# Kernel tuning notes

Hardware: AMD Instinct MI355X
Metric: run time of the kernel (lower is better)

## Reference

```python
import jax, jax.numpy as jnp
import numpy as np

EPS = 1e-9

def dice(x, alpha):
    # Dice: batch-norm over dim 0 (unbiased var, ddof=1), then gated blend.
    mu = jnp.mean(x, axis=0)
    var = jnp.var(x, axis=0, ddof=1)
    p = jax.nn.sigmoid((x - mu) / jnp.sqrt(var + EPS))
    return alpha * x * (1.0 - p) + x * p


def setup_inputs() -> dict:
    key = jax.random.key(0)
    ks = jax.random.split(key, 8)
    bs, seq, dim = 2048, 200, 64
    d_in = dim * 4
    return {
        "query": jax.random.normal(ks[0], (bs, dim), jnp.float32),
        "user_behavior": jax.random.normal(ks[1], (bs, seq, dim), jnp.float32),
        "mask": jax.random.uniform(ks[2], (bs, seq, 1), jnp.float32),
        "W1": jax.random.normal(ks[3], (d_in, 32), jnp.float32) / np.sqrt(d_in),
        "b1": jnp.zeros((32,), jnp.float32),
        "alpha1": jnp.zeros((1,), jnp.float32),
        "W2": jax.random.normal(ks[4], (32, 16), jnp.float32) / np.sqrt(32.0),
        "b2": jnp.zeros((16,), jnp.float32),
        "alpha2": jnp.zeros((1,), jnp.float32),
        "W3": jax.random.normal(ks[5], (16, 1), jnp.float32) / np.sqrt(16.0),
        "b3": jnp.zeros((1,), jnp.float32),
    }


def reference(query, user_behavior, mask, W1, b1, alpha1, W2, b2, alpha2, W3, b3):
    # query: (bs, dim) -> broadcast to (bs, seq, dim)
    q = jnp.broadcast_to(query[:, None, :], user_behavior.shape)
    attn_input = jnp.concatenate(
        [q, user_behavior, q - user_behavior, q * user_behavior], axis=-1
    )  # (bs, seq, 4*dim)
    h = dice(attn_input @ W1 + b1, alpha1)
    h = dice(h @ W2 + b2, alpha2)
    attns = h @ W3 + b3  # (bs, seq, 1)
    attns = attns * mask
    output = jnp.sum(user_behavior * attns, axis=1)  # (bs, dim)
    return output, attns
```

## Files before the change

kernel.cpp:

```cpp
#include <hip/hip_runtime.h>
#include <math.h>

#define BS  2048
#define SEQ 200
#define DIM 64
#define C1  32
#define C2  16

typedef __attribute__((ext_vector_type(8))) short bf16x8_t;
typedef __attribute__((ext_vector_type(4))) float f32x4_t;
typedef __attribute__((ext_vector_type(4))) short short4_t;

__device__ __forceinline__ float dice1(float x, float m, float r, float al) {
    float t = (x - m) * r;
    float p = 1.f / (1.f + __expf(-t));
    return x * (al + p * (1.f - al));
}

__device__ __forceinline__ unsigned short f2bf(float f) {
    union { float f; unsigned u; } a;
    a.f = f;
    unsigned r = a.u + 0x7fff + ((a.u >> 16) & 1);
    return (unsigned short)(r >> 16);
}

__global__ __launch_bounds__(256) void k_gemm1(const float* __restrict__ q,
                                               const float* __restrict__ ub,
                                               const float* __restrict__ W1,
                                               const float* __restrict__ b1,
                                               float* __restrict__ z1) {
    const int bs = blockIdx.x;
    const int tid = threadIdx.x;
    __shared__ __align__(16) short s_A[208 * 64];
    __shared__ __align__(16) short s_B[2 * 2 * 64 * 8];
    __shared__ __align__(16) float s_qw[C1];

    char* sAc = (char*)s_A;
    const float* qrow = q + bs * DIM;
    const float4* src4 = (const float4*)(ub + (size_t)bs * SEQ * DIM);

    float4 st[13];
    #pragma unroll
    for (int it = 0; it < 13; ++it) {
        int i = tid + it * 256;
        if (it < 12 || i < SEQ * 16) st[it] = src4[i];
        else { st[it].x = 0.f; st[it].y = 0.f; st[it].z = 0.f; st[it].w = 0.f; }
    }

    {
        const int kt = tid >> 7;
        const int nt = (tid >> 6) & 1;
        const int l  = tid & 63;
        const int c  = nt * 16 + (l & 15);
        bf16x8_t bfr;
        #pragma unroll
        for (int j = 0; j < 8; ++j) {
            int k = kt * 32 + ((l >> 4) << 3) + j;
            float wb = W1[(64 + k) * C1 + c] - W1[(128 + k) * C1 + c]
                     + qrow[k] * W1[(192 + k) * C1 + c];
            bfr[j] = (short)f2bf(wb);
        }
        *(bf16x8_t*)((char*)s_B + (((kt * 2 + nt) * 64) + l) * 16) = bfr;
    }
    if (tid < C1) {
        float a = b1[tid];
        #pragma unroll 8
        for (int d = 0; d < DIM; ++d)
            a = fmaf(qrow[d], W1[d * C1 + tid] + W1[(128 + d) * C1 + tid], a);
        s_qw[tid] = a;
    }

    #pragma unroll
    for (int it = 0; it < 13; ++it) {
        int i = tid + it * 256;
        int row = i >> 4, f4 = i & 15;
        int off = row * 128 + ((f4 * 8) ^ ((row & 7) << 4));
        short4_t u;
        u.x = (short)f2bf(st[it].x);
        u.y = (short)f2bf(st[it].y);
        u.z = (short)f2bf(st[it].z);
        u.w = (short)f2bf(st[it].w);
        *(short4_t*)(sAc + off) = u;
    }
    __syncthreads();

    const int wave = tid >> 6;
    const int l = tid & 63;
    const int g = l >> 4;
    const bf16x8_t b00 = *(const bf16x8_t*)((char*)s_B + (0 * 64 + l) * 16);
    const bf16x8_t b01 = *(const bf16x8_t*)((char*)s_B + (1 * 64 + l) * 16);
    const bf16x8_t b10 = *(const bf16x8_t*)((char*)s_B + (2 * 64 + l) * 16);
    const bf16x8_t b11 = *(const bf16x8_t*)((char*)s_B + (3 * 64 + l) * 16);
    const float qw0 = s_qw[l & 15];
    const float qw1 = s_qw[16 + (l & 15)];
    float* z1_b = z1 + (size_t)bs * SEQ * C1;

    for (int mt = wave; mt < 13; mt += 4) {
        const int row = mt * 16 + (l & 15);
        const int sw = (row & 7) << 4;
        bf16x8_t a0 = *(const bf16x8_t*)(sAc + row * 128 + ((g * 16) ^ sw));
        bf16x8_t a1 = *(const bf16x8_t*)(sAc + row * 128 + (((64 + g * 16)) ^ sw));
        f32x4_t acc0 = {0.f, 0.f, 0.f, 0.f};
        f32x4_t acc1 = {0.f, 0.f, 0.f, 0.f};
        acc0 = __builtin_amdgcn_mfma_f32_16x16x32_bf16(a0, b00, acc0, 0, 0, 0);
        acc0 = __builtin_amdgcn_mfma_f32_16x16x32_bf16(a1, b10, acc0, 0, 0, 0);
        acc1 = __builtin_amdgcn_mfma_f32_16x16x32_bf16(a0, b01, acc1, 0, 0, 0);
        acc1 = __builtin_amdgcn_mfma_f32_16x16x32_bf16(a1, b11, acc1, 0, 0, 0);
        const int orow = mt * 16 + g * 4;
        #pragma unroll
        for (int r = 0; r < 4; ++r) {
            int rr = orow + r;
            if (rr < SEQ) {
                z1_b[rr * C1 + (l & 15)]      = acc0[r] + qw0;
                z1_b[rr * C1 + 16 + (l & 15)] = acc1[r] + qw1;
            }
        }
    }
}

template <int C>
__global__ __launch_bounds__(256) void k_redA(const float* __restrict__ z,
                                              float* __restrict__ pS,
                                              float* __restrict__ pQ) {
    constexpr int Q = C / 4;
    constexpr int NG = 256 / Q;
    const int seq = blockIdx.x;
    const int part = blockIdx.y;
    const int cq = threadIdx.x % Q;
    const int g = threadIdx.x / Q;
    float4 s = {0.f, 0.f, 0.f, 0.f}, ss = {0.f, 0.f, 0.f, 0.f};
    const int b0 = part * 256;
    for (int b = b0 + g; b < b0 + 256; b += NG) {
        float4 v = *(const float4*)(z + ((size_t)b * SEQ + seq) * C + cq * 4);
        s.x += v.x; s.y += v.y; s.z += v.z; s.w += v.w;
        ss.x = fmaf(v.x, v.x, ss.x);
        ss.y = fmaf(v.y, v.y, ss.y);
        ss.z = fmaf(v.z, v.z, ss.z);
        ss.w = fmaf(v.w, v.w, ss.w);
    }
    __shared__ __align__(16) float4 sh_s[256];
    __shared__ __align__(16) float4 sh_q[256];
    sh_s[threadIdx.x] = s;
    sh_q[threadIdx.x] = ss;
    for (int h = NG / 2; h > 0; h >>= 1) {
        __syncthreads();
        if (g < h) {
            int o = threadIdx.x + h * Q;
            float4 s2 = sh_s[o], q2 = sh_q[o];
            s.x += s2.x; s.y += s2.y; s.z += s2.z; s.w += s2.w;
            ss.x += q2.x; ss.y += q2.y; ss.z += q2.z; ss.w += q2.w;
            sh_s[threadIdx.x] = s;
            sh_q[threadIdx.x] = ss;
        }
    }
    if (g == 0) {
        *(float4*)(pS + ((size_t)part * SEQ + seq) * C + cq * 4) = s;
        *(float4*)(pQ + ((size_t)part * SEQ + seq) * C + cq * 4) = ss;
    }
}

template <int C>
__global__ __launch_bounds__(64) void k_redB(const float* __restrict__ pS,
                                             const float* __restrict__ pQ,
                                             float* __restrict__ mu,
                                             float* __restrict__ rstd) {
    const int seq = blockIdx.x;
    const int c = threadIdx.x;
    if (c >= C) return;
    float s = 0.f, ss = 0.f;
    #pragma unroll
    for (int p = 0; p < 8; ++p) {
        s += pS[((size_t)p * SEQ + seq) * C + c];
        ss += pQ[((size_t)p * SEQ + seq) * C + c];
    }
    float m = s / (float)BS;
    float var = (ss - s * m) / (float)(BS - 1);
    mu[seq * C + c] = m;
    rstd[seq * C + c] = rsqrtf(var + 1e-9f);
}

__global__ __launch_bounds__(256) void k_gemm2(const float* __restrict__ z1,
                                               const float* __restrict__ mu1,
                                               const float* __restrict__ rstd1,
                                               const float* __restrict__ alpha1,
                                               const float* __restrict__ W2,
                                               const float* __restrict__ b2,
                                               float* __restrict__ z2) {
    const int tid = threadIdx.x;
    __shared__ __align__(16) float s_w2[C1 * C2];
    __shared__ float s_b2[C2];
    for (int i = tid; i < C1 * C2; i += 256) s_w2[i] = W2[i];
    if (tid < C2) s_b2[tid] = b2[tid];
    __syncthreads();
    const int gidx = blockIdx.x * 256 + tid;
    const int bsb = gidx / SEQ;
    const int seq = gidx - bsb * SEQ;
    const float al = alpha1[0];
    const float4* z4 = (const float4*)(z1 + (size_t)gidx * C1);
    const float4* m4 = (const float4*)(mu1 + seq * C1);
    const float4* r4 = (const float4*)(rstd1 + seq * C1);
    float h[C1];
    #pragma unroll
    for (int k = 0; k < C1 / 4; ++k) {
        float4 x = z4[k], m = m4[k], r = r4[k];
        h[k * 4 + 0] = dice1(x.x, m.x, r.x, al);
        h[k * 4 + 1] = dice1(x.y, m.y, r.y, al);
        h[k * 4 + 2] = dice1(x.z, m.z, r.z, al);
        h[k * 4 + 3] = dice1(x.w, m.w, r.w, al);
    }
    const float4* w4 = (const float4*)s_w2;
    float4 o[4];
    #pragma unroll
    for (int qd = 0; qd < 4; ++qd) {
        o[qd].x = s_b2[qd * 4 + 0];
        o[qd].y = s_b2[qd * 4 + 1];
        o[qd].z = s_b2[qd * 4 + 2];
        o[qd].w = s_b2[qd * 4 + 3];
    }
    #pragma unroll
    for (int c = 0; c < C1; ++c) {
        float hc = h[c];
        #pragma unroll
        for (int qd = 0; qd < 4; ++qd) {
            float4 w = w4[c * 4 + qd];
            o[qd].x = fmaf(hc, w.x, o[qd].x);
            o[qd].y = fmaf(hc, w.y, o[qd].y);
            o[qd].z = fmaf(hc, w.z, o[qd].z);
            o[qd].w = fmaf(hc, w.w, o[qd].w);
        }
    }
    float4* outp = (float4*)(z2 + (size_t)gidx * C2);
    #pragma unroll
    for (int qd = 0; qd < 4; ++qd) outp[qd] = o[qd];
}

__global__ __launch_bounds__(256) void k_final(const float* __restrict__ z2,
                                               const float* __restrict__ mu2,
                                               const float* __restrict__ rstd2,
                                               const float* __restrict__ alpha2,
                                               const float* __restrict__ W3,
                                               const float* __restrict__ b3,
                                               const float* __restrict__ mask,
                                               const float* __restrict__ ub,
                                               float* __restrict__ out,
                                               float* __restrict__ attns) {
    const int bs = blockIdx.x;
    const int tid = threadIdx.x;
    __shared__ float s_attn[SEQ];
    __shared__ float s_w3[C2];
    __shared__ __align__(16) float4 s_pool[256];
    if (tid < C2) s_w3[tid] = W3[tid];
    __syncthreads();
    if (tid < SEQ) {
        const float al = alpha2[0];
        const float bb3 = b3[0];
        const float4* z4 = (const float4*)(z2 + ((size_t)bs * SEQ + tid) * C2);
        const float4* m4 = (const float4*)(mu2 + tid * C2);
        const float4* r4 = (const float4*)(rstd2 + tid * C2);
        float a = bb3;
        #pragma unroll
        for (int k = 0; k < C2 / 4; ++k) {
            float4 x = z4[k], m = m4[k], r = r4[k];
            a = fmaf(dice1(x.x, m.x, r.x, al), s_w3[k * 4 + 0], a);
            a = fmaf(dice1(x.y, m.y, r.y, al), s_w3[k * 4 + 1], a);
            a = fmaf(dice1(x.z, m.z, r.z, al), s_w3[k * 4 + 2], a);
            a = fmaf(dice1(x.w, m.w, r.w, al), s_w3[k * 4 + 3], a);
        }
        a *= mask[bs * SEQ + tid];
        s_attn[tid] = a;
        attns[(size_t)bs * SEQ + tid] = a;
    }
    __syncthreads();
    const int dq = tid & 15;
    const int sg = tid >> 4;
    float4 acc = {0.f, 0.f, 0.f, 0.f};
    const float4* ub4 = (const float4*)(ub + (size_t)bs * SEQ * DIM);
    for (int s = sg; s < SEQ; s += 16) {
        float a = s_attn[s];
        float4 v = ub4[s * 16 + dq];
        acc.x = fmaf(v.x, a, acc.x);
        acc.y = fmaf(v.y, a, acc.y);
        acc.z = fmaf(v.z, a, acc.z);
        acc.w = fmaf(v.w, a, acc.w);
    }
    s_pool[tid] = acc;
    for (int h = 8; h > 0; h >>= 1) {
        __syncthreads();
        if (sg < h) {
            float4 o = s_pool[tid + h * 16];
            acc.x += o.x; acc.y += o.y; acc.z += o.z; acc.w += o.w;
            s_pool[tid] = acc;
        }
    }
    if (sg == 0)
        *(float4*)(out + (size_t)bs * DIM + dq * 4) = acc;
}

extern "C" void kernel_launch(void* const* d_in, const int* in_sizes, int n_in,
                              void* d_out, int out_size, void* d_ws, size_t ws_size,
                              hipStream_t stream) {
    const float* q    = (const float*)d_in[0];
    const float* ub   = (const float*)d_in[1];
    const float* mask = (const float*)d_in[2];
    const float* W1   = (const float*)d_in[3];
    const float* b1   = (const float*)d_in[4];
    const float* a1   = (const float*)d_in[5];
    const float* W2   = (const float*)d_in[6];
    const float* b2   = (const float*)d_in[7];
    const float* a2   = (const float*)d_in[8];
    const float* W3   = (const float*)d_in[9];
    const float* b3   = (const float*)d_in[10];

    float* out   = (float*)d_out;
    float* attns = out + (size_t)BS * DIM;

    float* ws = (float*)d_ws;
    float* z1 = ws;
    float* z2 = z1 + (size_t)BS * SEQ * C1;
    float* mu1   = z2 + (size_t)BS * SEQ * C2;
    float* rstd1 = mu1 + SEQ * C1;
    float* mu2   = rstd1 + SEQ * C1;
    float* rstd2 = mu2 + SEQ * C2;
    float* pS    = attns;
    float* pQ    = pS + 8 * SEQ * C1;

    hipLaunchKernelGGL(k_gemm1, dim3(BS), dim3(256), 0, stream, q, ub, W1, b1, z1);
    hipLaunchKernelGGL((k_redA<C1>), dim3(SEQ, 8), dim3(256), 0, stream, z1, pS, pQ);
    hipLaunchKernelGGL((k_redB<C1>), dim3(SEQ), dim3(64), 0, stream, pS, pQ, mu1, rstd1);
    hipLaunchKernelGGL(k_gemm2, dim3(BS * SEQ / 256), dim3(256), 0, stream, z1, mu1, rstd1, a1, W2, b2, z2);
    hipLaunchKernelGGL((k_redA<C2>), dim3(SEQ, 8), dim3(256), 0, stream, z2, pS, pQ);
    hipLaunchKernelGGL((k_redB<C2>), dim3(SEQ), dim3(64), 0, stream, pS, pQ, mu2, rstd2);
    hipLaunchKernelGGL(k_final, dim3(BS), dim3(256), 0, stream, z2, mu2, rstd2, a2, W3, b3, mask, ub, out, attns);
}
```

Baseline: 272.7 us.

## Store intermediates in bf16, fuse layer-2 GEMM with stat reductions, drop LDS staging

Intermediates z1 and z2 are now stored as bf16 instead of fp32, halving the traffic of the reduction and GEMM passes that re-read them. k_gemm1 reads user_behavior straight from global memory into MFMA fragments and writes its output tile through LDS with coalesced stores. The second GEMM moves to MFMA and is fused with the finalize step for layer-1 statistics and the partial sums for layer-2 statistics, which removes two kernel launches and one full pass over z2. In exchange, rounding to bf16 before the batch-norm statistics adds precision risk, and the gemm2 grid of 200 blocks is small and may underfill the GPU.

```diff
diff --git a/kernel.cpp b/kernel.cpp
--- a/kernel.cpp
+++ b/kernel.cpp
@@ -9,7 +9,6 @@
 
 typedef __attribute__((ext_vector_type(8))) short bf16x8_t;
 typedef __attribute__((ext_vector_type(4))) float f32x4_t;
-typedef __attribute__((ext_vector_type(4))) short short4_t;
 
 __device__ __forceinline__ float dice1(float x, float m, float r, float al) {
     float t = (x - m) * r;
@@ -24,28 +23,24 @@
     return (unsigned short)(r >> 16);
 }
 
+__device__ __forceinline__ float bf2f(short h) {
+    union { unsigned u; float f; } a;
+    a.u = ((unsigned)(unsigned short)h) << 16;
+    return a.f;
+}
+
 __global__ __launch_bounds__(256) void k_gemm1(const float* __restrict__ q,
                                                const float* __restrict__ ub,
                                                const float* __restrict__ W1,
                                                const float* __restrict__ b1,
-                                               float* __restrict__ z1) {
+                                               short* __restrict__ z1) {
     const int bs = blockIdx.x;
     const int tid = threadIdx.x;
-    __shared__ __align__(16) short s_A[208 * 64];
     __shared__ __align__(16) short s_B[2 * 2 * 64 * 8];
     __shared__ __align__(16) float s_qw[C1];
-
-    char* sAc = (char*)s_A;
+    __shared__ __align__(16) short s_z[208 * C1];
+
     const float* qrow = q + bs * DIM;
-    const float4* src4 = (const float4*)(ub + (size_t)bs * SEQ * DIM);
-
-    float4 st[13];
-    #pragma unroll
-    for (int it = 0; it < 13; ++it) {
-        int i = tid + it * 256;
-        if (it < 12 || i < SEQ * 16) st[it] = src4[i];
-        else { st[it].x = 0.f; st[it].y = 0.f; st[it].z = 0.f; st[it].w = 0.f; }
-    }
 
     {
         const int kt = tid >> 7;
@@ -68,19 +63,6 @@
         for (int d = 0; d < DIM; ++d)
             a = fmaf(qrow[d], W1[d * C1 + tid] + W1[(128 + d) * C1 + tid], a);
         s_qw[tid] = a;
-    }
-
-    #pragma unroll
-    for (int it = 0; it < 13; ++it) {
-        int i = tid + it * 256;
-        int row = i >> 4, f4 = i & 15;
-        int off = row * 128 + ((f4 * 8) ^ ((row & 7) << 4));
-        short4_t u;
-        u.x = (short)f2bf(st[it].x);
-        u.y = (short)f2bf(st[it].y);
-        u.z = (short)f2bf(st[it].z);
-        u.w = (short)f2bf(st[it].w);
-        *(short4_t*)(sAc + off) = u;
     }
     __syncthreads();
 
@@ -93,13 +75,25 @@
     const bf16x8_t b11 = *(const bf16x8_t*)((char*)s_B + (3 * 64 + l) * 16);
     const float qw0 = s_qw[l & 15];
     const float qw1 = s_qw[16 + (l & 15)];
-    float* z1_b = z1 + (size_t)bs * SEQ * C1;
+    const float* ubb = ub + (size_t)bs * SEQ * DIM;
 
     for (int mt = wave; mt < 13; mt += 4) {
-        const int row = mt * 16 + (l & 15);
-        const int sw = (row & 7) << 4;
-        bf16x8_t a0 = *(const bf16x8_t*)(sAc + row * 128 + ((g * 16) ^ sw));
-        bf16x8_t a1 = *(const bf16x8_t*)(sAc + row * 128 + (((64 + g * 16)) ^ sw));
+        int row = mt * 16 + (l & 15);
+        int rc = row > SEQ - 1 ? SEQ - 1 : row;
+        const float* rp = ubb + rc * DIM + g * 8;
+        float4 f0 = *(const float4*)(rp);
+        float4 f1 = *(const float4*)(rp + 4);
+        float4 f2 = *(const float4*)(rp + 32);
+        float4 f3 = *(const float4*)(rp + 36);
+        bf16x8_t a0, a1;
+        a0[0] = (short)f2bf(f0.x); a0[1] = (short)f2bf(f0.y);
+        a0[2] = (short)f2bf(f0.z); a0[3] = (short)f2bf(f0.w);
+        a0[4] = (short)f2bf(f1.x); a0[5] = (short)f2bf(f1.y);
+        a0[6] = (short)f2bf(f1.z); a0[7] = (short)f2bf(f1.w);
+        a1[0] = (short)f2bf(f2.x); a1[1] = (short)f2bf(f2.y);
+        a1[2] = (short)f2bf(f2.z); a1[3] = (short)f2bf(f2.w);
+        a1[4] = (short)f2bf(f3.x); a1[5] = (short)f2bf(f3.y);
+        a1[6] = (short)f2bf(f3.z); a1[7] = (short)f2bf(f3.w);
         f32x4_t acc0 = {0.f, 0.f, 0.f, 0.f};
         f32x4_t acc1 = {0.f, 0.f, 0.f, 0.f};
         acc0 = __builtin_amdgcn_mfma_f32_16x16x32_bf16(a0, b00, acc0, 0, 0, 0);
@@ -109,132 +103,157 @@
         const int orow = mt * 16 + g * 4;
         #pragma unroll
         for (int r = 0; r < 4; ++r) {
-            int rr = orow + r;
-            if (rr < SEQ) {
-                z1_b[rr * C1 + (l & 15)]      = acc0[r] + qw0;
-                z1_b[rr * C1 + 16 + (l & 15)] = acc1[r] + qw1;
-            }
-        }
-    }
-}
-
-template <int C>
-__global__ __launch_bounds__(256) void k_redA(const float* __restrict__ z,
-                                              float* __restrict__ pS,
-                                              float* __restrict__ pQ) {
-    constexpr int Q = C / 4;
-    constexpr int NG = 256 / Q;
+            s_z[(orow + r) * C1 + (l & 15)]      = (short)f2bf(acc0[r] + qw0);
+            s_z[(orow + r) * C1 + 16 + (l & 15)] = (short)f2bf(acc1[r] + qw1);
+        }
+    }
+    __syncthreads();
+    bf16x8_t* dst = (bf16x8_t*)(z1 + (size_t)bs * SEQ * C1);
+    const bf16x8_t* srcl = (const bf16x8_t*)s_z;
+    for (int i = tid; i < SEQ * C1 / 8; i += 256) dst[i] = srcl[i];
+}
+
+__global__ __launch_bounds__(256) void k_redA1(const short* __restrict__ z1,
+                                               float* __restrict__ pS,
+                                               float* __restrict__ pQ) {
     const int seq = blockIdx.x;
     const int part = blockIdx.y;
-    const int cq = threadIdx.x % Q;
-    const int g = threadIdx.x / Q;
-    float4 s = {0.f, 0.f, 0.f, 0.f}, ss = {0.f, 0.f, 0.f, 0.f};
-    const int b0 = part * 256;
-    for (int b = b0 + g; b < b0 + 256; b += NG) {
-        float4 v = *(const float4*)(z + ((size_t)b * SEQ + seq) * C + cq * 4);
-        s.x += v.x; s.y += v.y; s.z += v.z; s.w += v.w;
-        ss.x = fmaf(v.x, v.x, ss.x);
-        ss.y = fmaf(v.y, v.y, ss.y);
-        ss.z = fmaf(v.z, v.z, ss.z);
-        ss.w = fmaf(v.w, v.w, ss.w);
-    }
-    __shared__ __align__(16) float4 sh_s[256];
-    __shared__ __align__(16) float4 sh_q[256];
-    sh_s[threadIdx.x] = s;
-    sh_q[threadIdx.x] = ss;
-    for (int h = NG / 2; h > 0; h >>= 1) {
-        __syncthreads();
-        if (g < h) {
-            int o = threadIdx.x + h * Q;
-            float4 s2 = sh_s[o], q2 = sh_q[o];
-            s.x += s2.x; s.y += s2.y; s.z += s2.z; s.w += s2.w;
-            ss.x += q2.x; ss.y += q2.y; ss.z += q2.z; ss.w += q2.w;
-            sh_s[threadIdx.x] = s;
-            sh_q[threadIdx.x] = ss;
-        }
-    }
-    if (g == 0) {
-        *(float4*)(pS + ((size_t)part * SEQ + seq) * C + cq * 4) = s;
-        *(float4*)(pQ + ((size_t)part * SEQ + seq) * C + cq * 4) = ss;
-    }
-}
-
-template <int C>
-__global__ __launch_bounds__(64) void k_redB(const float* __restrict__ pS,
-                                             const float* __restrict__ pQ,
-                                             float* __restrict__ mu,
-                                             float* __restrict__ rstd) {
-    const int seq = blockIdx.x;
-    const int c = threadIdx.x;
-    if (c >= C) return;
-    float s = 0.f, ss = 0.f;
+    const int tid = threadIdx.x;
+    const int cq = tid & 3;
+    float s[8], qq[8];
+    #pragma unroll
+    for (int j = 0; j < 8; ++j) { s[j] = 0.f; qq[j] = 0.f; }
+    #pragma unroll
+    for (int it = 0; it < 4; ++it) {
+        int b = part * 256 + (tid >> 2) + it * 64;
+        bf16x8_t v = *(const bf16x8_t*)(z1 + ((size_t)b * SEQ + seq) * C1 + cq * 8);
+        #pragma unroll
+        for (int j = 0; j < 8; ++j) {
+            float f = bf2f(v[j]);
+            s[j] += f;
+            qq[j] = fmaf(f, f, qq[j]);
+        }
+    }
+    #pragma unroll
+    for (int st = 4; st <= 32; st <<= 1) {
+        #pragma unroll
+        for (int j = 0; j < 8; ++j) {
+            s[j]  += __shfl_xor(s[j],  st);
+            qq[j] += __shfl_xor(qq[j], st);
+        }
+    }
+    __shared__ float shS[4][4][8], shQ[4][4][8];
+    const int wave = tid >> 6, l = tid & 63;
+    if (l < 4) {
+        #pragma unroll
+        for (int j = 0; j < 8; ++j) { shS[wave][l][j] = s[j]; shQ[wave][l][j] = qq[j]; }
+    }
+    __syncthreads();
+    if (tid < 32) {
+        int c4 = tid >> 3, j = tid & 7;
+        float a = shS[0][c4][j] + shS[1][c4][j] + shS[2][c4][j] + shS[3][c4][j];
+        float b = shQ[0][c4][j] + shQ[1][c4][j] + shQ[2][c4][j] + shQ[3][c4][j];
+        pS[((size_t)part * SEQ + seq) * C1 + c4 * 8 + j] = a;
+        pQ[((size_t)part * SEQ + seq) * C1 + c4 * 8 + j] = b;
+    }
+}
+
+__global__ __launch_bounds__(256) void k_gemm2s(const short* __restrict__ z1,
+                                                const float* __restrict__ pS1,
+                                                const float* __restrict__ pQ1,
+                                                const float* __restrict__ alpha1,
+                                                const float* __restrict__ W2,
+                                                const float* __restrict__ b2,
+                                                short* __restrict__ z2,
+                                                float* __restrict__ pS2,
+                                                float* __restrict__ pQ2) {
+    const int strip = blockIdx.x;
+    const int part = blockIdx.y;
+    const int tid = threadIdx.x;
+    __shared__ float s_mu[8][C1];
+    __shared__ float s_rs[8][C1];
+
+    {
+        int ss = tid >> 5, c = tid & 31;
+        int seqg = strip * 8 + ss;
+        float s = 0.f, q = 0.f;
+        #pragma unroll
+        for (int p = 0; p < 8; ++p) {
+            s += pS1[((size_t)p * SEQ + seqg) * C1 + c];
+            q += pQ1[((size_t)p * SEQ + seqg) * C1 + c];
+        }
+        float m = s / (float)BS;
+        float var = (q - s * m) / (float)(BS - 1);
+        s_mu[ss][c] = m;
+        s_rs[ss][c] = rsqrtf(var + 1e-9f);
+    }
+    const int wave = tid >> 6;
+    const int l = tid & 63;
+    const int g = l >> 4;
+    const int cB = l & 15;
+    bf16x8_t bw;
+    #pragma unroll
+    for (int j = 0; j < 8; ++j) bw[j] = (short)f2bf(W2[(g * 8 + j) * C2 + cB]);
+    const float bias = b2[cB];
+    const float al = alpha1[0];
+    __syncthreads();
+
+    const int cb = (l & 3) * 8;
+    const int srcLane = (l & 15) * 4 + g;
+    for (int sq = wave * 2; sq < wave * 2 + 2; ++sq) {
+        const int seqg = strip * 8 + sq;
+        float sumS = 0.f, sumQ = 0.f;
+        for (int t = 0; t < 16; ++t) {
+            const int b0 = part * 256 + t * 16;
+            const int brow = b0 + (l >> 2);
+            bf16x8_t zv = *(const bf16x8_t*)(z1 + ((size_t)brow * SEQ + seqg) * C1 + cb);
+            union { bf16x8_t v; int w[4]; } hp;
+            #pragma unroll
+            for (int j = 0; j < 8; ++j) {
+                float x = bf2f(zv[j]);
+                hp.v[j] = (short)f2bf(dice1(x, s_mu[sq][cb + j], s_rs[sq][cb + j], al));
+            }
+            union { bf16x8_t v; int w[4]; } af;
+            #pragma unroll
+            for (int w4 = 0; w4 < 4; ++w4) af.w[w4] = __shfl(hp.w[w4], srcLane);
+            f32x4_t acc = {bias, bias, bias, bias};
+            acc = __builtin_amdgcn_mfma_f32_16x16x32_bf16(af.v, bw, acc, 0, 0, 0);
+            #pragma unroll
+            for (int r = 0; r < 4; ++r) {
+                int rb = b0 + g * 4 + r;
+                z2[((size_t)rb * SEQ + seqg) * C2 + cB] = (short)f2bf(acc[r]);
+                sumS += acc[r];
+                sumQ = fmaf(acc[r], acc[r], sumQ);
+            }
+        }
+        sumS += __shfl_xor(sumS, 16); sumS += __shfl_xor(sumS, 32);
+        sumQ += __shfl_xor(sumQ, 16); sumQ += __shfl_xor(sumQ, 32);
+        if (l < 16) {
+            pS2[((size_t)part * SEQ + seqg) * C2 + cB] = sumS;
+            pQ2[((size_t)part * SEQ + seqg) * C2 + cB] = sumQ;
+        }
+    }
+}
+
+__global__ __launch_bounds__(64) void k_redB2(const float* __restrict__ pS,
+                                              const float* __restrict__ pQ,
+                                              float* __restrict__ mu,
+                                              float* __restrict__ rstd) {
+    const int cell = blockIdx.x * 64 + threadIdx.x;
+    const int seq = cell >> 4, c = cell & 15;
+    float s = 0.f, q = 0.f;
     #pragma unroll
     for (int p = 0; p < 8; ++p) {
-        s += pS[((size_t)p * SEQ + seq) * C + c];
-        ss += pQ[((size_t)p * SEQ + seq) * C + c];
+        s += pS[((size_t)p * SEQ + seq) * C2 + c];
+        q += pQ[((size_t)p * SEQ + seq) * C2 + c];
     }
     float m = s / (float)BS;
-    float var = (ss - s * m) / (float)(BS - 1);
-    mu[seq * C + c] = m;
-    rstd[seq * C + c] = rsqrtf(var + 1e-9f);
-}
-
-__global__ __launch_bounds__(256) void k_gemm2(const float* __restrict__ z1,
-                                               const float* __restrict__ mu1,
-                                               const float* __restrict__ rstd1,
-                                               const float* __restrict__ alpha1,
-                                               const float* __restrict__ W2,
-                                               const float* __restrict__ b2,
-                                               float* __restrict__ z2) {
-    const int tid = threadIdx.x;
-    __shared__ __align__(16) float s_w2[C1 * C2];
-    __shared__ float s_b2[C2];
-    for (int i = tid; i < C1 * C2; i += 256) s_w2[i] = W2[i];
-    if (tid < C2) s_b2[tid] = b2[tid];
-    __syncthreads();
-    const int gidx = blockIdx.x * 256 + tid;
-    const int bsb = gidx / SEQ;
-    const int seq = gidx - bsb * SEQ;
-    const float al = alpha1[0];
-    const float4* z4 = (const float4*)(z1 + (size_t)gidx * C1);
-    const float4* m4 = (const float4*)(mu1 + seq * C1);
-    const float4* r4 = (const float4*)(rstd1 + seq * C1);
-    float h[C1];
-    #pragma unroll
-    for (int k = 0; k < C1 / 4; ++k) {
-        float4 x = z4[k], m = m4[k], r = r4[k];
-        h[k * 4 + 0] = dice1(x.x, m.x, r.x, al);
-        h[k * 4 + 1] = dice1(x.y, m.y, r.y, al);
-        h[k * 4 + 2] = dice1(x.z, m.z, r.z, al);
-        h[k * 4 + 3] = dice1(x.w, m.w, r.w, al);
-    }
-    const float4* w4 = (const float4*)s_w2;
-    float4 o[4];
-    #pragma unroll
-    for (int qd = 0; qd < 4; ++qd) {
-        o[qd].x = s_b2[qd * 4 + 0];
-        o[qd].y = s_b2[qd * 4 + 1];
-        o[qd].z = s_b2[qd * 4 + 2];
-        o[qd].w = s_b2[qd * 4 + 3];
-    }
-    #pragma unroll
-    for (int c = 0; c < C1; ++c) {
-        float hc = h[c];
-        #pragma unroll
-        for (int qd = 0; qd < 4; ++qd) {
-            float4 w = w4[c * 4 + qd];
-            o[qd].x = fmaf(hc, w.x, o[qd].x);
-            o[qd].y = fmaf(hc, w.y, o[qd].y);
-            o[qd].z = fmaf(hc, w.z, o[qd].z);
-            o[qd].w = fmaf(hc, w.w, o[qd].w);
-        }
-    }
-    float4* outp = (float4*)(z2 + (size_t)gidx * C2);
-    #pragma unroll
-    for (int qd = 0; qd < 4; ++qd) outp[qd] = o[qd];
-}
-
-__global__ __launch_bounds__(256) void k_final(const float* __restrict__ z2,
+    float var = (q - s * m) / (float)(BS - 1);
+    mu[seq * C2 + c] = m;
+    rstd[seq * C2 + c] = rsqrtf(var + 1e-9f);
+}
+
+__global__ __launch_bounds__(256) void k_final(const short* __restrict__ z2,
                                                const float* __restrict__ mu2,
                                                const float* __restrict__ rstd2,
                                                const float* __restrict__ alpha2,
@@ -254,17 +273,22 @@
     if (tid < SEQ) {
         const float al = alpha2[0];
         const float bb3 = b3[0];
-        const float4* z4 = (const float4*)(z2 + ((size_t)bs * SEQ + tid) * C2);
+        bf16x8_t v0 = *(const bf16x8_t*)(z2 + ((size_t)bs * SEQ + tid) * C2);
+        bf16x8_t v1 = *(const bf16x8_t*)(z2 + ((size_t)bs * SEQ + tid) * C2 + 8);
         const float4* m4 = (const float4*)(mu2 + tid * C2);
         const float4* r4 = (const float4*)(rstd2 + tid * C2);
         float a = bb3;
         #pragma unroll
-        for (int k = 0; k < C2 / 4; ++k) {
-            float4 x = z4[k], m = m4[k], r = r4[k];
-            a = fmaf(dice1(x.x, m.x, r.x, al), s_w3[k * 4 + 0], a);
-            a = fmaf(dice1(x.y, m.y, r.y, al), s_w3[k * 4 + 1], a);
-            a = fmaf(dice1(x.z, m.z, r.z, al), s_w3[k * 4 + 2], a);
-            a = fmaf(dice1(x.w, m.w, r.w, al), s_w3[k * 4 + 3], a);
+        for (int k = 0; k < 4; ++k) {
+            float4 m = m4[k], r = r4[k];
+            float x0 = bf2f(k < 2 ? v0[k * 4 + 0] : v1[(k - 2) * 4 + 0]);
+            float x1 = bf2f(k < 2 ? v0[k * 4 + 1] : v1[(k - 2) * 4 + 1]);
+            float x2 = bf2f(k < 2 ? v0[k * 4 + 2] : v1[(k - 2) * 4 + 2]);
+            float x3 = bf2f(k < 2 ? v0[k * 4 + 3] : v1[(k - 2) * 4 + 3]);
+            a = fmaf(dice1(x0, m.x, r.x, al), s_w3[k * 4 + 0], a);
+            a = fmaf(dice1(x1, m.y, r.y, al), s_w3[k * 4 + 1], a);
+            a = fmaf(dice1(x2, m.z, r.z, al), s_w3[k * 4 + 2], a);
+            a = fmaf(dice1(x3, m.w, r.w, al), s_w3[k * 4 + 3], a);
         }
         a *= mask[bs * SEQ + tid];
         s_attn[tid] = a;
@@ -315,20 +339,21 @@
     float* attns = out + (size_t)BS * DIM;
 
     float* ws = (float*)d_ws;
-    float* z1 = ws;
-    float* z2 = z1 + (size_t)BS * SEQ * C1;
-    float* mu1   = z2 + (size_t)BS * SEQ * C2;
-    float* rstd1 = mu1 + SEQ * C1;
-    float* mu2   = rstd1 + SEQ * C1;
+    short* z1 = (short*)ws;
+    short* z2 = z1 + (size_t)BS * SEQ * C1;
+    float* fw = (float*)(z2 + (size_t)BS * SEQ * C2);
+    float* pS1 = fw;
+    float* pQ1 = pS1 + 8 * SEQ * C1;
+    float* pS2 = pQ1 + 8 * SEQ * C1;
+    float* pQ2 = pS2 + 8 * SEQ * C2;
+    float* mu2   = pQ2 + 8 * SEQ * C2;
     float* rstd2 = mu2 + SEQ * C2;
-    float* pS    = attns;
-    float* pQ    = pS + 8 * SEQ * C1;
 
     hipLaunchKernelGGL(k_gemm1, dim3(BS), dim3(256), 0, stream, q, ub, W1, b1, z1);
-    hipLaunchKernelGGL((k_redA<C1>), dim3(SEQ, 8), dim3(256), 0, stream, z1, pS, pQ);
-    hipLaunchKernelGGL((k_redB<C1>), dim3(SEQ), dim3(64), 0, stream, pS, pQ, mu1, rstd1);
-    hipLaunchKernelGGL(k_gemm2, dim3(BS * SEQ / 256), dim3(256), 0, stream, z1, mu1, rstd1, a1, W2, b2, z2);
-    hipLaunchKernelGGL((k_redA<C2>), dim3(SEQ, 8), dim3(256), 0, stream, z2, pS, pQ);
-    hipLaunchKernelGGL((k_redB<C2>), dim3(SEQ), dim3(64), 0, stream, pS, pQ, mu2, rstd2);
-    hipLaunchKernelGGL(k_final, dim3(BS), dim3(256), 0, stream, z2, mu2, rstd2, a2, W3, b3, mask, ub, out, attns);
-}
+    hipLaunchKernelGGL(k_redA1, dim3(SEQ, 8), dim3(256), 0, stream, z1, pS1, pQ1);
+    hipLaunchKernelGGL(k_gemm2s, dim3(25, 8), dim3(256), 0, stream,
+                       z1, pS1, pQ1, a1, W2, b2, z2, pS2, pQ2);
+    hipLaunchKernelGGL(k_redB2, dim3(50), dim3(64), 0, stream, pS2, pQ2, mu2, rstd2);
+    hipLaunchKernelGGL(k_final, dim3(BS), dim3(256), 0, stream,
+                       z2, mu2, rstd2, a2, W3, b3, mask, ub, out, attns);
+}
```

Measured after the change: 249.8 us. 8.4% less time.
